# Performance work log

Hardware: AMD Instinct MI355X
Metric: run time of the kernel (lower is better)

## Reference

```python
import jax, jax.numpy as jnp
import numpy as np

L = 4        # num_blocks
D = 512      # d_model
H = 8        # num_heads
DFF = 2048   # d_ff
EPS = 1.1920929e-07  # torch RMSNorm default eps = finfo(fp32).eps


def setup_inputs() -> dict:
    key = jax.random.key(0)
    ks = jax.random.split(key, 12)
    B, S = 4, 1024
    s = 0.02
    return {
        "x": jax.random.normal(ks[0], (B, S, D), jnp.float32),
        "col_ids": jax.random.randint(ks[1], (B, S), 0, 32),
        "row_ids": jax.random.randint(ks[2], (B, S), 0, 128),
        "nbr_ids": jax.random.randint(ks[3], (B, S), 0, 64),
        # per-block, per-relation attention weights (nn.Linear: y = x @ W.T)
        "Wq": jax.random.normal(ks[4], (L, 4, D, D), jnp.float32) * s,
        "Wk": jax.random.normal(ks[5], (L, 4, D, D), jnp.float32) * s,
        "Wv": jax.random.normal(ks[6], (L, 4, D, D), jnp.float32) * s,
        "Wo": jax.random.normal(ks[7], (L, 4, D, D), jnp.float32) * s,
        # SwiGLU FFN weights per block
        "W1": jax.random.normal(ks[8], (L, DFF, D), jnp.float32) * s,
        "W3": jax.random.normal(ks[9], (L, DFF, D), jnp.float32) * s,
        "W2": jax.random.normal(ks[10], (L, D, DFF), jnp.float32) * s,
        # RMSNorm scales: 4 attn norms + 1 ffn norm per block + final norm_out
        "g_attn": jnp.ones((L, 4, D), jnp.float32),
        "g_ffn": jnp.ones((L, D), jnp.float32),
        "g_out": jnp.ones((D,), jnp.float32),
    }


def _rms(x, g):
    return x * jax.lax.rsqrt(jnp.mean(x * x, axis=-1, keepdims=True) + EPS) * g


def _attn(x, wq, wk, wv, wo, mask):
    # x: [B,S,D]; mask: [B,S,S] bool (True = attend) or None for full attention
    B, S, _ = x.shape
    hd = D // H
    scale = 1.0 / np.sqrt(hd).astype(np.float32)
    q = (x @ wq.T).reshape(B, S, H, hd).transpose(0, 2, 1, 3)  # bhsd
    k = (x @ wk.T).reshape(B, S, H, hd).transpose(0, 2, 1, 3)
    v = (x @ wv.T).reshape(B, S, H, hd).transpose(0, 2, 1, 3)
    sc = jnp.einsum('bhqd,bhkd->bhqk', q, k) * scale
    if mask is not None:
        sc = jnp.where(mask[:, None, :, :], sc, jnp.float32(-1e30))
    a = jax.nn.softmax(sc, axis=-1)
    o = jnp.einsum('bhqk,bhkd->bhqd', a, v).transpose(0, 2, 1, 3).reshape(B, S, D)
    return o @ wo.T


def reference(x, col_ids, row_ids, nbr_ids, Wq, Wk, Wv, Wo, W1, W3, W2, g_attn, g_ffn, g_out):
    # relation order in RelationalBlock: col, feat, nbr, full
    masks = [ids[:, :, None] == ids[:, None, :] for ids in (col_ids, row_ids, nbr_ids)] + [None]
    for l in range(L):
        for r in range(4):
            x = x + _attn(_rms(x, g_attn[l, r]), Wq[l, r], Wk[l, r], Wv[l, r], Wo[l, r], masks[r])
        h = _rms(x, g_ffn[l])
        x = x + (jax.nn.silu(h @ W1[l].T) * (h @ W3[l].T)) @ W2[l].T
    return _rms(x, g_out)
```

## Files before the change

kernel.cpp:

```cpp
#include <hip/hip_runtime.h>
#include <hip/hip_bf16.h>


typedef __attribute__((ext_vector_type(4))) float f32x4;
typedef __attribute__((ext_vector_type(8))) short s16x8;
typedef __attribute__((ext_vector_type(4))) short s16x4;

#define SEQ 1024
#define DM 512
#define MTOT 4096
#define EPSV 1.1920929e-07f
#define LOG2E 1.44269504088896f

static __device__ __forceinline__ float b2f(short s) {
  unsigned u = ((unsigned)(unsigned short)s) << 16;
  return __builtin_bit_cast(float, u);
}
static __device__ __forceinline__ short f2b(float f) {
  unsigned u = __builtin_bit_cast(unsigned, f);
  u = (u + 0x7fffu + ((u >> 16) & 1u)) >> 16;
  return (short)(unsigned short)u;
}

#define MFMA_BF16(a, b, c) __builtin_amdgcn_mfma_f32_16x16x32_bf16((a), (b), (c), 0, 0, 0)
#define GLLDS(gp, lp)                                                                        \
  __builtin_amdgcn_global_load_lds((const __attribute__((address_space(1))) unsigned*)(gp),  \
                                   (__attribute__((address_space(3))) unsigned*)(lp), 16, 0, 0)
#define GLLDS4(gp, lp)                                                                       \
  __builtin_amdgcn_global_load_lds((const __attribute__((address_space(1))) unsigned*)(gp),  \
                                   (__attribute__((address_space(3))) unsigned*)(lp), 4, 0, 0)

__global__ void cvt_all(const f32x4* __restrict__ wq, const f32x4* __restrict__ wk,
                        const f32x4* __restrict__ wv, const f32x4* __restrict__ wo,
                        const f32x4* __restrict__ w1, const f32x4* __restrict__ w3,
                        const f32x4* __restrict__ w2, const float* __restrict__ g_attn,
                        const float* __restrict__ g_ffn, s16x4* __restrict__ wqkv,
                        s16x4* __restrict__ wob, s16x4* __restrict__ w13,
                        s16x4* __restrict__ w2b) {
  int i = blockIdx.x * 256 + threadIdx.x;
  int which = blockIdx.y;
  s16x4 o;
  if (which < 3) {
    const f32x4* src = which == 0 ? wq : (which == 1 ? wk : wv);
    f32x4 v = src[i];
    int lr = i >> 16, k4 = i & 127, n = (i >> 7) & 511;
    const float* gp = g_attn + lr * 512 + k4 * 4;
    float sc = (which == 0) ? 0.125f * LOG2E : 1.0f;
#pragma unroll
    for (int j = 0; j < 4; j++) o[j] = f2b(v[j] * gp[j] * sc);
    wqkv[(size_t)lr * 196608 + (which * 512 + n) * 128 + k4] = o;
  } else if (which == 3) {
    f32x4 v = wo[i];
#pragma unroll
    for (int j = 0; j < 4; j++) o[j] = f2b(v[j]);
    wob[i] = o;
  } else if (which < 6) {
    const f32x4* src = which == 4 ? w1 : w3;
    int off = which - 4;
    f32x4 v = src[i];
    int l = i >> 18, n = (i >> 7) & 2047, k4 = i & 127;
    const float* gp = g_ffn + l * 512 + k4 * 4;
#pragma unroll
    for (int j = 0; j < 4; j++) o[j] = f2b(v[j] * gp[j]);
    w13[(size_t)l * 524288 + (n * 2 + off) * 128 + k4] = o;
  } else {
    f32x4 v = w2[i];
#pragma unroll
    for (int j = 0; j < 4; j++) o[j] = f2b(v[j]);
    w2b[i] = o;
  }
}

__global__ void init_kernel(const float* __restrict__ xin, float* __restrict__ x,
                            short* __restrict__ h, float* __restrict__ ssq) {
  int row = blockIdx.x * 4 + (threadIdx.x >> 6);
  int lane = threadIdx.x & 63;
  const float* xr = xin + (size_t)row * DM + lane * 8;
  f32x4 a = *(const f32x4*)xr;
  f32x4 b = *(const f32x4*)(xr + 4);
  float* xo = x + (size_t)row * DM + lane * 8;
  *(f32x4*)xo = a;
  *(f32x4*)(xo + 4) = b;
  s16x8 ho;
#pragma unroll
  for (int j = 0; j < 4; j++) { ho[j] = f2b(a[j]); ho[4 + j] = f2b(b[j]); }
  *(s16x8*)(h + (size_t)row * DM + lane * 8) = ho;
  float ss = a[0]*a[0]+a[1]*a[1]+a[2]*a[2]+a[3]*a[3]+b[0]*b[0]+b[1]*b[1]+b[2]*b[2]+b[3]*b[3];
#pragma unroll
  for (int m = 1; m < 64; m <<= 1) ss += __shfl_xor(ss, m, 64);
  if (lane == 0) ssq[row] = ss;
}

__global__ void rmsnorm_out(const float* __restrict__ x, const float* __restrict__ g,
                            float* __restrict__ outp) {
  int row = blockIdx.x * 4 + (threadIdx.x >> 6);
  int lane = threadIdx.x & 63;
  const float* xr = x + (size_t)row * DM + lane * 8;
  f32x4 a = *(const f32x4*)xr;
  f32x4 b = *(const f32x4*)(xr + 4);
  float ss = a[0]*a[0]+a[1]*a[1]+a[2]*a[2]+a[3]*a[3]+b[0]*b[0]+b[1]*b[1]+b[2]*b[2]+b[3]*b[3];
#pragma unroll
  for (int m = 1; m < 64; m <<= 1) ss += __shfl_xor(ss, m, 64);
  float sc = rsqrtf(ss * (1.0f / DM) + EPSV);
  const float* gp = g + lane * 8;
  float* o = outp + (size_t)row * DM + lane * 8;
  f32x4 o0, o1;
#pragma unroll
  for (int j = 0; j < 4; j++) { o0[j] = a[j] * sc * gp[j]; o1[j] = b[j] * sc * gp[4 + j]; }
  *(f32x4*)o = o0;
  *(f32x4*)(o + 4) = o1;
}

template<int AR, int AC, int FUSE>
__global__ __launch_bounds__(256) void gemm_bt(const short* __restrict__ A, const short* __restrict__ W,
                                               short* __restrict__ outb, float* __restrict__ outf,
                                               short* __restrict__ vtb,
                                               const float* __restrict__ ssq_in,
                                               float* __restrict__ ssq_out,
                                               short* __restrict__ hb, int N, int K) {
  constexpr int BM = AR * 32;
  constexpr int BN = AC * 32;
  constexpr int NA = BM / 64, NB = BN / 64;
  constexpr int LPS = NA + NB;
  __shared__ short As[2][BM * 32];
  __shared__ short Bs[2][BN * 32];
  const int tid = threadIdx.x;
  const int lane = tid & 63;
  const int w = tid >> 6;
  const int wr = w >> 1, wc = w & 1;
  const int qi = lane & 15, g = lane >> 4;
  const int m0 = blockIdx.x * BM, n0 = blockIdx.y * BN;

  const short* ap[NA];
  const short* wp[NB];
#pragma unroll
  for (int i = 0; i < NA; i++) {
    int s = i * 256 + tid;
    int row = s >> 2, gl = s & 3, gd = gl ^ ((row >> 1) & 3);
    ap[i] = A + (size_t)(m0 + row) * K + gd * 8;
  }
#pragma unroll
  for (int i = 0; i < NB; i++) {
    int s = i * 256 + tid;
    int row = s >> 2, gl = s & 3, gd = gl ^ ((row >> 1) & 3);
    wp[i] = W + (size_t)(n0 + row) * K + gd * 8;
  }
  int aro[AR], bro[AC];
#pragma unroll
  for (int i = 0; i < AR; i++) {
    int row = wr * AR * 16 + i * 16 + qi;
    aro[i] = row * 64 + ((g ^ ((row >> 1) & 3)) * 16);
  }
#pragma unroll
  for (int j = 0; j < AC; j++) {
    int row = wc * AC * 16 + j * 16 + qi;
    bro[j] = row * 64 + ((g ^ ((row >> 1) & 3)) * 16);
  }
  f32x4 acc[AR][AC] = {};

#define STAGE_G(BUF)                                                             \
  {                                                                              \
    _Pragma("unroll")                                                            \
    for (int i = 0; i < NA; i++) {                                               \
      GLLDS(ap[i], (char*)As[BUF] + (i * 256 + w * 64) * 16);                    \
      ap[i] += 32;                                                               \
    }                                                                            \
    _Pragma("unroll")                                                            \
    for (int i = 0; i < NB; i++) {                                               \
      GLLDS(wp[i], (char*)Bs[BUF] + (i * 256 + w * 64) * 16);                    \
      wp[i] += 32;                                                               \
    }                                                                            \
  }

#define BODY_G(BUF, T)                                                           \
  {                                                                              \
    s16x8 af[AR], bf[AC];                                                        \
    _Pragma("unroll")                                                            \
    for (int i = 0; i < AR; i++) af[i] = *(const s16x8*)((char*)As[BUF] + aro[i]); \
    _Pragma("unroll")                                                            \
    for (int j = 0; j < AC; j++) bf[j] = *(const s16x8*)((char*)Bs[BUF] + bro[j]); \
    asm volatile("s_waitcnt lgkmcnt(0)" ::: "memory");                           \
    __builtin_amdgcn_s_barrier();                                                \
    bool more = ((T) + 2 < nt);                                                  \
    if (more) STAGE_G(BUF);                                                      \
    _Pragma("unroll")                                                            \
    for (int i = 0; i < AR; i++)                                                 \
      _Pragma("unroll")                                                          \
      for (int j = 0; j < AC; j++)                                               \
        acc[i][j] = MFMA_BF16(af[i], bf[j], acc[i][j]);                          \
    if (more) asm volatile("s_waitcnt vmcnt(%0)" :: "n"(LPS) : "memory");        \
    else      asm volatile("s_waitcnt vmcnt(0)" ::: "memory");                   \
    __builtin_amdgcn_s_barrier();                                                \
  }

  const int nt = K >> 5;
  STAGE_G(0);
  STAGE_G(1);
  asm volatile("s_waitcnt vmcnt(%0)" :: "n"(LPS) : "memory");
  __builtin_amdgcn_s_barrier();
  for (int t = 0; t < nt; t += 2) {
    BODY_G(0, t);
    BODY_G(1, t + 1);
  }
#undef STAGE_G
#undef BODY_G

  float srow[AR][4];
  if (FUSE == 2 || FUSE == 3) {
#pragma unroll
    for (int i = 0; i < AR; i++) {
      int rbase = m0 + wr * AR * 16 + i * 16 + g * 4;
#pragma unroll
      for (int r = 0; r < 4; r++)
        srow[i][r] = rsqrtf(ssq_in[rbase + r] * (1.0f / DM) + EPSV);
    }
  }
  float part[AR][4];
  if (FUSE == 1) {
#pragma unroll
    for (int i = 0; i < AR; i++)
#pragma unroll
      for (int r = 0; r < 4; r++) part[i][r] = 0.f;
  }

#pragma unroll
  for (int i = 0; i < AR; i++) {
    int rbase = m0 + wr * AR * 16 + i * 16 + g * 4;
#pragma unroll
    for (int j = 0; j < AC; j++) {
      int col = n0 + wc * AC * 16 + j * 16 + qi;
      if (FUSE == 2 && col >= 1024) {
        int bbv = rbase >> 10, s = rbase & 1023;
        int c = col - 1024, hhv = c >> 6, d = c & 63;
        int o = (s & 63) >> 2;
        int gg = o & 3, h2 = (o >> 2) & 1, q32 = o >> 3;
        int pnew = q32 * 8 + gg * 2 + h2;
        s16x4 o4;
#pragma unroll
        for (int r = 0; r < 4; r++) o4[r] = f2b(acc[i][j][r] * srow[i][r]);
        *(s16x4*)(vtb + (((size_t)(bbv * 8 + hhv) * 64 + d) << 10) + (s & ~63) + pnew * 4) = o4;
      } else if (FUSE == 3) {
#pragma unroll
        for (int r = 0; r < 4; r++) {
          float own = acc[i][j][r] * srow[i][r];
          float other = __shfl_xor(own, 1, 64);
          float sv = own / (1.0f + __expf(-own));
          if (!(lane & 1))
            outb[(size_t)(rbase + r) * (N >> 1) + (col >> 1)] = f2b(sv * other);
        }
      } else if (FUSE == 1) {
#pragma unroll
        for (int r = 0; r < 4; r++) {
          size_t idx = (size_t)(rbase + r) * N + col;
          float xnew = outf[idx] + acc[i][j][r];
          outf[idx] = xnew;
          hb[idx] = f2b(xnew);
          part[i][r] += xnew * xnew;
        }
      } else {
#pragma unroll
        for (int r = 0; r < 4; r++)
          outb[(size_t)(rbase + r) * N + col] = f2b(acc[i][j][r] * srow[i][r]);
      }
    }
  }
  if (FUSE == 1) {
#pragma unroll
    for (int i = 0; i < AR; i++) {
      int rbase = m0 + wr * AR * 16 + i * 16 + g * 4;
#pragma unroll
      for (int r = 0; r < 4; r++) {
        float p = part[i][r];
#pragma unroll
        for (int m = 1; m < 16; m <<= 1) p += __shfl_xor(p, m, 16);
        if (qi == 0) atomicAdd(&ssq_out[rbase + r], p);
      }
    }
  }
}

__global__ __launch_bounds__(256) void attn_kernel(const short* __restrict__ qkv, const short* __restrict__ vt,
                                                   const int* __restrict__ ids, short* __restrict__ Ob) {
  const int bh = blockIdx.x;
  const int bb = bh >> 3, hh = bh & 7;
  const int q0 = blockIdx.y * 64;
  const int tid = threadIdx.x, lane = tid & 63, w = tid >> 6;
  const int g = lane >> 4, qi = lane & 15;
  __shared__ short Kl[2][128 * 64];
  __shared__ short Vl[2][64 * 128];
  __shared__ int Kid[2][128];
  const short* kbase = qkv + 512 + hh * 64;
  const short* vbase = vt + (size_t)bh * 64 * SEQ;
  s16x8 qf0, qf1;
  {
    int qrow = q0 + w * 16 + qi;
    const short* qp = qkv + (size_t)(bb * SEQ + qrow) * 1536 + hh * 64 + g * 8;
    qf0 = *(const s16x8*)qp;
    qf1 = *(const s16x8*)(qp + 32);
  }
  int qid = 0;
  if (ids) qid = ids[bb * SEQ + q0 + w * 16 + qi];
  float m_ = -1e30f, l_ = 0.f;
  f32x4 oacc[4] = {};

#define STAGE_ATTN(buf, ktt)                                                                     \
  {                                                                                              \
    _Pragma("unroll")                                                                            \
    for (int i = 0; i < 4; i++) {                                                                \
      int s = i * 256 + tid;                                                                     \
      int row = s >> 3, gl = s & 7, gd = gl ^ (row & 7);                                         \
      GLLDS(kbase + (size_t)(bb * SEQ + (ktt) + row) * 1536 + gd * 8,                            \
            (char*)Kl[buf] + (i * 256 + w * 64) * 16);                                           \
    }                                                                                            \
    _Pragma("unroll")                                                                            \
    for (int i = 0; i < 4; i++) {                                                                \
      int s = i * 256 + tid;                                                                     \
      int d = s >> 4, gl = s & 15, gd = gl ^ (d & 7);                                            \
      GLLDS(vbase + (size_t)d * SEQ + (ktt) + gd * 8, (char*)Vl[buf] + (i * 256 + w * 64) * 16); \
    }                                                                                            \
    if (ids && w < 2) GLLDS4(ids + bb * SEQ + (ktt) + w * 64 + lane, (char*)Kid[buf] + w * 256); \
  }

  STAGE_ATTN(0, 0);
  __syncthreads();
  int cur = 0;
  for (int kt = 0; kt < SEQ; kt += 128) {
    if (kt + 128 < SEQ) STAGE_ATTN(cur ^ 1, kt + 128);
    f32x4 sc[8];
#pragma unroll
    for (int kc = 0; kc < 8; kc++) {
      int krow = kc * 16 + qi;
      s16x8 kf0 = *(const s16x8*)(Kl[cur] + krow * 64 + ((g ^ (krow & 7)) * 8));
      s16x8 kf1 = *(const s16x8*)(Kl[cur] + krow * 64 + (((4 + g) ^ (krow & 7)) * 8));
      f32x4 s4 = {};
      s4 = MFMA_BF16(kf0, qf0, s4);
      s4 = MFMA_BF16(kf1, qf1, s4);
      sc[kc] = s4;
    }
    float p[8][4];
#pragma unroll
    for (int kc = 0; kc < 8; kc++)
#pragma unroll
      for (int r = 0; r < 4; r++) p[kc][r] = sc[kc][r];
    if (ids) {
#pragma unroll
      for (int kc = 0; kc < 8; kc++) {
        int4 kid4 = *(const int4*)(Kid[cur] + kc * 16 + g * 4);
        if (kid4.x != qid) p[kc][0] = -1e30f;
        if (kid4.y != qid) p[kc][1] = -1e30f;
        if (kid4.z != qid) p[kc][2] = -1e30f;
        if (kid4.w != qid) p[kc][3] = -1e30f;
      }
    }
    float mx = fmaxf(fmaxf(p[0][0], p[0][1]), fmaxf(p[0][2], p[0][3]));
#pragma unroll
    for (int kc = 1; kc < 8; kc++)
      mx = fmaxf(mx, fmaxf(fmaxf(p[kc][0], p[kc][1]), fmaxf(p[kc][2], p[kc][3])));
    mx = fmaxf(mx, __shfl_xor(mx, 16, 64));
    mx = fmaxf(mx, __shfl_xor(mx, 32, 64));
    if (__any(mx > m_ + 8.f)) {
      float nm = fmaxf(m_, mx);
      float c = exp2f(m_ - nm);
      m_ = nm;
      l_ *= c;
#pragma unroll
      for (int r = 0; r < 4; r++) {
        float cr = __shfl(c, g * 4 + r, 16);
        oacc[0][r] *= cr; oacc[1][r] *= cr; oacc[2][r] *= cr; oacc[3][r] *= cr;
      }
    }
    float sum = 0.f;
#pragma unroll
    for (int kc = 0; kc < 8; kc++)
#pragma unroll
      for (int r = 0; r < 4; r++) {
        p[kc][r] = exp2f(p[kc][r] - m_);
        sum += p[kc][r];
      }
    sum += __shfl_xor(sum, 16, 64);
    sum += __shfl_xor(sum, 32, 64);
    l_ += sum;
#pragma unroll
    for (int kk = 0; kk < 2; kk++) {
      s16x8 pa, pb;
#pragma unroll
      for (int r = 0; r < 4; r++) {
        pa[r] = f2b(p[kk * 4 + 0][r]); pa[4 + r] = f2b(p[kk * 4 + 1][r]);
        pb[r] = f2b(p[kk * 4 + 2][r]); pb[4 + r] = f2b(p[kk * 4 + 3][r]);
      }
#pragma unroll
      for (int dt = 0; dt < 4; dt++) {
        int dl = dt * 16 + qi;
        const short* vr = Vl[cur] + dl * 128;
        s16x8 vf0 = *(const s16x8*)(vr + (kk * 8 + (g ^ (dl & 7))) * 8);
        s16x8 vf1 = *(const s16x8*)(vr + (kk * 8 + ((4 + g) ^ (dl & 7))) * 8);
        oacc[dt] = MFMA_BF16(pa, vf0, oacc[dt]);
        oacc[dt] = MFMA_BF16(pb, vf1, oacc[dt]);
      }
    }
    __syncthreads();
    cur ^= 1;
  }
#undef STAGE_ATTN
  const size_t obase = (size_t)(bb * SEQ) * DM + hh * 64;
#pragma unroll
  for (int r = 0; r < 4; r++) {
    float lr = __shfl(l_, g * 4 + r, 16);
    float inv = 1.0f / lr;
    int q = q0 + w * 16 + g * 4 + r;
#pragma unroll
    for (int dt = 0; dt < 4; dt++)
      Ob[obase + (size_t)q * DM + dt * 16 + qi] = f2b(oacc[dt][r] * inv);
  }
}

extern "C" void kernel_launch(void* const* d_in, const int* in_sizes, int n_in,
                              void* d_out, int out_size, void* d_ws, size_t ws_size,
                              hipStream_t stream) {
  const float* x_in  = (const float*)d_in[0];
  const int* col_ids = (const int*)d_in[1];
  const int* row_ids = (const int*)d_in[2];
  const int* nbr_ids = (const int*)d_in[3];
  const float* g_attn = (const float*)d_in[11];
  const float* g_ffn  = (const float*)d_in[12];
  const float* g_out  = (const float*)d_in[13];

  char* ws = (char*)d_ws;
  float* x    = (float*)(ws);
  short* h    = (short*)(ws + (size_t)(8u  << 20));
  short* qkv  = (short*)(ws + (size_t)(12u << 20));
  short* vt   = (short*)(ws + (size_t)(24u << 20));
  short* ob   = (short*)(ws + (size_t)(28u << 20));
  float* sbuf = (float*)(ws + (size_t)(33u << 20));
  short* fa   = (short*)(ws + (size_t)(44u << 20));
  short* wqkv = (short*)(ws + (size_t)(60u  << 20));
  short* wob  = (short*)(ws + (size_t)(84u  << 20));
  short* w13  = (short*)(ws + (size_t)(92u  << 20));
  short* w2b  = (short*)(ws + (size_t)(108u << 20));

  hipMemsetAsync(sbuf, 0, 21 * 4096 * sizeof(float), stream);
  cvt_all<<<dim3(4096, 7), 256, 0, stream>>>((const f32x4*)d_in[4], (const f32x4*)d_in[5],
                                             (const f32x4*)d_in[6], (const f32x4*)d_in[7],
                                             (const f32x4*)d_in[8], (const f32x4*)d_in[9],
                                             (const f32x4*)d_in[10], g_attn, g_ffn,
                                             (s16x4*)wqkv, (s16x4*)wob, (s16x4*)w13, (s16x4*)w2b);
  init_kernel<<<1024, 256, 0, stream>>>(x_in, x, h, sbuf);

  const int* idsarr[4] = {col_ids, row_ids, nbr_ids, nullptr};

  for (int l = 0; l < 4; l++) {
    for (int r = 0; r < 4; r++) {
      int slot = l * 5 + r;
      size_t woff = (size_t)(l * 4 + r) * 1536 * DM;
      gemm_bt<4, 2, 2><<<dim3(32, 24), 256, 0, stream>>>(h, wqkv + woff, qkv, nullptr, vt,
                                                         sbuf + (size_t)slot * 4096, nullptr,
                                                         nullptr, 1536, DM);
      attn_kernel<<<dim3(32, 16), 256, 0, stream>>>(qkv, vt, idsarr[r], ob);
      gemm_bt<2, 2, 1><<<dim3(64, 8), 256, 0, stream>>>(ob, wob + (size_t)(l * 4 + r) * DM * DM,
                                                        nullptr, x, nullptr, nullptr,
                                                        sbuf + (size_t)(slot + 1) * 4096, h, DM, DM);
    }
    int fslot = l * 5 + 4;
    gemm_bt<4, 2, 3><<<dim3(32, 64), 256, 0, stream>>>(h, w13 + (size_t)l * 4096 * DM, fa, nullptr,
                                                       nullptr, sbuf + (size_t)fslot * 4096,
                                                       nullptr, nullptr, 4096, DM);
    gemm_bt<2, 2, 1><<<dim3(64, 8), 256, 0, stream>>>(fa, w2b + (size_t)l * DM * 2048, nullptr, x,
                                                      nullptr, nullptr,
                                                      sbuf + (size_t)(fslot + 1) * 4096, h, DM, 2048);
  }
  rmsnorm_out<<<1024, 256, 0, stream>>>(x, g_out, (float*)d_out);
}
```

Baseline: 1.134 ms.

## Widen weight conversion with nontemporal I/O, fold memset into init, add MFMA priority hints

The weight conversion kernel now has each thread handle four float4 chunks, using nontemporal loads and 32-byte nontemporal stores, and launches a quarter as many blocks. The separate hipMemsetAsync of the sum-of-squares buffer is removed and the zeroing moved into init_kernel, which saves one launch. The attention kernel wraps its MFMA sections in s_setprio hints to favour matrix issue. The wider per-thread work in conversion lowers occupancy, and the priority hints may or may not help scheduling.

```diff
diff --git a/kernel.cpp b/kernel.cpp
--- a/kernel.cpp
+++ b/kernel.cpp
@@ -5,6 +5,7 @@
 typedef __attribute__((ext_vector_type(4))) float f32x4;
 typedef __attribute__((ext_vector_type(8))) short s16x8;
 typedef __attribute__((ext_vector_type(4))) short s16x4;
+typedef __attribute__((ext_vector_type(16))) short s16x16;
 
 #define SEQ 1024
 #define DM 512
@@ -34,45 +35,56 @@
                         const f32x4* __restrict__ wv, const f32x4* __restrict__ wo,
                         const f32x4* __restrict__ w1, const f32x4* __restrict__ w3,
                         const f32x4* __restrict__ w2, const float* __restrict__ g_attn,
-                        const float* __restrict__ g_ffn, s16x4* __restrict__ wqkv,
-                        s16x4* __restrict__ wob, s16x4* __restrict__ w13,
-                        s16x4* __restrict__ w2b) {
-  int i = blockIdx.x * 256 + threadIdx.x;
+                        const float* __restrict__ g_ffn, short* __restrict__ wqkv,
+                        short* __restrict__ wob, short* __restrict__ w13,
+                        short* __restrict__ w2b) {
+  int i0 = (blockIdx.x * 256 + threadIdx.x) * 4;
   int which = blockIdx.y;
-  s16x4 o;
+  s16x16 o;
   if (which < 3) {
     const f32x4* src = which == 0 ? wq : (which == 1 ? wk : wv);
-    f32x4 v = src[i];
-    int lr = i >> 16, k4 = i & 127, n = (i >> 7) & 511;
+    f32x4 v[4];
+#pragma unroll
+    for (int c = 0; c < 4; c++) v[c] = __builtin_nontemporal_load(&src[i0 + c]);
+    int lr = i0 >> 16, k4 = i0 & 127, n = (i0 >> 7) & 511;
     const float* gp = g_attn + lr * 512 + k4 * 4;
     float sc = (which == 0) ? 0.125f * LOG2E : 1.0f;
 #pragma unroll
-    for (int j = 0; j < 4; j++) o[j] = f2b(v[j] * gp[j] * sc);
-    wqkv[(size_t)lr * 196608 + (which * 512 + n) * 128 + k4] = o;
-  } else if (which == 3) {
-    f32x4 v = wo[i];
-#pragma unroll
-    for (int j = 0; j < 4; j++) o[j] = f2b(v[j]);
-    wob[i] = o;
-  } else if (which < 6) {
+    for (int c = 0; c < 4; c++)
+#pragma unroll
+      for (int j = 0; j < 4; j++) o[c * 4 + j] = f2b(v[c][j] * gp[c * 4 + j] * sc);
+    __builtin_nontemporal_store(o, (s16x16*)(wqkv + ((size_t)lr * 196608 + (which * 512 + n) * 128 + k4) * 4));
+  } else if (which == 3 || which == 6) {
+    const f32x4* src = which == 3 ? wo : w2;
+    short* dst = which == 3 ? wob : w2b;
+    f32x4 v[4];
+#pragma unroll
+    for (int c = 0; c < 4; c++) v[c] = __builtin_nontemporal_load(&src[i0 + c]);
+#pragma unroll
+    for (int c = 0; c < 4; c++)
+#pragma unroll
+      for (int j = 0; j < 4; j++) o[c * 4 + j] = f2b(v[c][j]);
+    __builtin_nontemporal_store(o, (s16x16*)(dst + (size_t)i0 * 4));
+  } else {
     const f32x4* src = which == 4 ? w1 : w3;
     int off = which - 4;
-    f32x4 v = src[i];
-    int l = i >> 18, n = (i >> 7) & 2047, k4 = i & 127;
+    f32x4 v[4];
+#pragma unroll
+    for (int c = 0; c < 4; c++) v[c] = __builtin_nontemporal_load(&src[i0 + c]);
+    int l = i0 >> 18, n = (i0 >> 7) & 2047, k4 = i0 & 127;
     const float* gp = g_ffn + l * 512 + k4 * 4;
 #pragma unroll
-    for (int j = 0; j < 4; j++) o[j] = f2b(v[j] * gp[j]);
-    w13[(size_t)l * 524288 + (n * 2 + off) * 128 + k4] = o;
-  } else {
-    f32x4 v = w2[i];
-#pragma unroll
-    for (int j = 0; j < 4; j++) o[j] = f2b(v[j]);
-    w2b[i] = o;
+    for (int c = 0; c < 4; c++)
+#pragma unroll
+      for (int j = 0; j < 4; j++) o[c * 4 + j] = f2b(v[c][j] * gp[c * 4 + j]);
+    __builtin_nontemporal_store(o, (s16x16*)(w13 + ((size_t)l * 524288 + (n * 2 + off) * 128 + k4) * 4));
   }
 }
 
 __global__ void init_kernel(const float* __restrict__ xin, float* __restrict__ x,
-                            short* __restrict__ h, float* __restrict__ ssq) {
+                            short* __restrict__ h, float* __restrict__ sbuf) {
+  int gid = blockIdx.x * 256 + threadIdx.x;
+  if (gid < 20 * 4096) sbuf[4096 + gid] = 0.f;
   int row = blockIdx.x * 4 + (threadIdx.x >> 6);
   int lane = threadIdx.x & 63;
   const float* xr = xin + (size_t)row * DM + lane * 8;
@@ -88,7 +100,7 @@
   float ss = a[0]*a[0]+a[1]*a[1]+a[2]*a[2]+a[3]*a[3]+b[0]*b[0]+b[1]*b[1]+b[2]*b[2]+b[3]*b[3];
 #pragma unroll
   for (int m = 1; m < 64; m <<= 1) ss += __shfl_xor(ss, m, 64);
-  if (lane == 0) ssq[row] = ss;
+  if (lane == 0) sbuf[row] = ss;
 }
 
 __global__ void rmsnorm_out(const float* __restrict__ x, const float* __restrict__ g,
@@ -327,6 +339,7 @@
   for (int kt = 0; kt < SEQ; kt += 128) {
     if (kt + 128 < SEQ) STAGE_ATTN(cur ^ 1, kt + 128);
     f32x4 sc[8];
+    __builtin_amdgcn_s_setprio(1);
 #pragma unroll
     for (int kc = 0; kc < 8; kc++) {
       int krow = kc * 16 + qi;
@@ -337,6 +350,7 @@
       s4 = MFMA_BF16(kf1, qf1, s4);
       sc[kc] = s4;
     }
+    __builtin_amdgcn_s_setprio(0);
     float p[8][4];
 #pragma unroll
     for (int kc = 0; kc < 8; kc++)
@@ -388,6 +402,7 @@
         pa[r] = f2b(p[kk * 4 + 0][r]); pa[4 + r] = f2b(p[kk * 4 + 1][r]);
         pb[r] = f2b(p[kk * 4 + 2][r]); pb[4 + r] = f2b(p[kk * 4 + 3][r]);
       }
+      __builtin_amdgcn_s_setprio(1);
 #pragma unroll
       for (int dt = 0; dt < 4; dt++) {
         int dl = dt * 16 + qi;
@@ -397,6 +412,7 @@
         oacc[dt] = MFMA_BF16(pa, vf0, oacc[dt]);
         oacc[dt] = MFMA_BF16(pb, vf1, oacc[dt]);
       }
+      __builtin_amdgcn_s_setprio(0);
     }
     __syncthreads();
     cur ^= 1;
@@ -438,12 +454,11 @@
   short* w13  = (short*)(ws + (size_t)(92u  << 20));
   short* w2b  = (short*)(ws + (size_t)(108u << 20));
 
-  hipMemsetAsync(sbuf, 0, 21 * 4096 * sizeof(float), stream);
-  cvt_all<<<dim3(4096, 7), 256, 0, stream>>>((const f32x4*)d_in[4], (const f32x4*)d_in[5],
+  cvt_all<<<dim3(1024, 7), 256, 0, stream>>>((const f32x4*)d_in[4], (const f32x4*)d_in[5],
                                              (const f32x4*)d_in[6], (const f32x4*)d_in[7],
                                              (const f32x4*)d_in[8], (const f32x4*)d_in[9],
                                              (const f32x4*)d_in[10], g_attn, g_ffn,
-                                             (s16x4*)wqkv, (s16x4*)wob, (s16x4*)w13, (s16x4*)w2b);
+                                             wqkv, wob, w13, w2b);
   init_kernel<<<1024, 256, 0, stream>>>(x_in, x, h, sbuf);
 
   const int* idsarr[4] = {col_ids, row_ids, nbr_ids, nullptr};
```

After: 1.276 ms. +12.5%, slower.
